# Performance work log

Measured on AMD Instinct MI355X. Metric: run time of the kernel, lower is better.

The kernel has to match this reference:

```python
import jax, jax.numpy as jnp
import numpy as np

B_, L, DM = 4, 1024, 1024
DI, DS, DR, DC = 1024, 16, 64, 4
NH = 4
DK = DM // NH


def setup_inputs() -> dict:
    key = jax.random.key(0)
    ks = jax.random.split(key, 16)
    def w(i, shape, scale=0.02):
        return jax.random.normal(ks[i], shape, dtype=jnp.float32) * scale
    inp = {
        "x": jax.random.normal(ks[0], (B_, L, DM), dtype=jnp.float32),
        "xx": jax.random.normal(ks[1], (B_, L, DI), dtype=jnp.float32),
        "in_proj_w": w(2, (DI, DM)),
        "conv_w": w(3, (DI, 1, DC)),            # depthwise conv, groups=DI
        "conv_b": jnp.zeros((DI,), jnp.float32),
        "x_proj_w": w(4, (DR + 2 * DS, DI)),
        "dt_proj_w": w(5, (DI, DR)),
        "dt_proj_b": jnp.zeros((DI,), jnp.float32),
        "A_log": jnp.log(jnp.tile(jnp.arange(1, DS + 1, dtype=jnp.float32)[None, :], (DI, 1))),
        "D": jnp.ones((DI,), jnp.float32),
        "wq": w(6, (DM, DM)), "bq": jnp.zeros((DM,), jnp.float32),
        "wk": w(7, (DM, DM)), "bk": jnp.zeros((DM,), jnp.float32),
        "wv": w(8, (DM, DM)), "bv": jnp.zeros((DM,), jnp.float32),
        "wo": w(9, (DM, DM)), "bo": jnp.zeros((DM,), jnp.float32),
    }
    return inp


def _stim_forward(x, xx, in_proj_w, conv_w, conv_b, x_proj_w, dt_proj_w, dt_proj_b,
                  A_log, D, wq, bq, wk, bk, wv, bv, wo, bo):
    b, l, _ = xx.shape
    # query branch: in_proj (Linear, no bias)
    q = x @ in_proj_w.T                                    # (b, l, DI)
    # kv branch: causal depthwise conv1d (padding d_conv-1, truncated to l)
    xc = jnp.transpose(xx, (0, 2, 1))                      # (b, DI, l)
    xc = jax.lax.conv_general_dilated(
        xc, conv_w, window_strides=(1,), padding=[(DC - 1, 0)],
        dimension_numbers=("NCH", "OIH", "NCH"), feature_group_count=DI)
    xc = xc + conv_b[None, :, None]
    u = jax.nn.silu(jnp.transpose(xc, (0, 2, 1)))          # (b, l, DI)
    # SSM parameter projections
    A = -jnp.exp(A_log)                                    # (DI, DS)
    x_dbl = u @ x_proj_w.T                                 # (b, l, DR+2*DS)
    delta, Bm, Cm = jnp.split(x_dbl, [DR, DR + DS], axis=-1)
    delta = jax.nn.softplus(delta @ dt_proj_w.T + dt_proj_b)  # (b, l, DI)
    deltaA = jnp.exp(jnp.einsum("bld,dn->bldn", delta, A))    # (b, l, DI, DS)
    deltaBu = jnp.einsum("bld,bln,bld->bldn", delta, Bm, u)   # (b, l, DI, DS)
    # selective scan over time
    def step(h, inp):
        dA_t, dBu_t, C_t = inp
        h = dA_t * h + dBu_t                               # (b, DI, DS)
        y_t = jnp.einsum("bdn,bn->bd", h, C_t)             # (b, DI)
        return h, y_t
    h0 = jnp.zeros((b, DI, DS), dtype=u.dtype)
    _, ys = jax.lax.scan(step, h0, (jnp.moveaxis(deltaA, 1, 0),
                                    jnp.moveaxis(deltaBu, 1, 0),
                                    jnp.moveaxis(Cm, 1, 0)))
    y = jnp.moveaxis(ys, 0, 1) + u * D                     # (b, l, DI)
    # cross attention: query = q, key/value = y
    Q = (q @ wq.T + bq).reshape(b, l, NH, DK).transpose(0, 2, 1, 3)
    K = (y @ wk.T + bk).reshape(b, l, NH, DK).transpose(0, 2, 1, 3)
    V = (y @ wv.T + bv).reshape(b, l, NH, DK).transpose(0, 2, 1, 3)
    scale = 1.0 / np.sqrt(DK).astype(np.float32)
    scores = jnp.einsum("bhqd,bhkd->bhqk", Q, K) * scale
    attn = jax.nn.softmax(scores, axis=-1)
    out = jnp.einsum("bhqk,bhkd->bhqd", attn, V)
    out = out.transpose(0, 2, 1, 3).reshape(b, l, DM)
    return out @ wo.T + bo


def reference(x, xx, in_proj_w, conv_w, conv_b, x_proj_w, dt_proj_w, dt_proj_b,
              A_log, D, wq, bq, wk, bk, wv, bv, wo, bo):
    return _stim_forward(x, xx, in_proj_w, conv_w, conv_b, x_proj_w, dt_proj_w,
                         dt_proj_b, A_log, D, wq, bq, wk, bk, wv, bv, wo, bo)
```

## Files before the change

kernel.cpp:

```cpp
#include <hip/hip_runtime.h>
#include <math.h>

#define B_  4
#define L_  1024
#define DM  1024
#define DI  1024
#define DS  16
#define DR  64
#define DCV 4
#define NH  4
#define DK  256

#define NCH 32
#define CHL (L_ / NCH)

typedef __attribute__((ext_vector_type(8))) short short8;
typedef __attribute__((ext_vector_type(4))) float floatx4;

static __device__ __forceinline__ unsigned short f2bf(float f) {
    unsigned int u = __float_as_uint(f);
    u += 0x7fffu + ((u >> 16) & 1u);
    return (unsigned short)(u >> 16);
}
static __device__ __forceinline__ float bf2f(unsigned short s) {
    return __uint_as_float(((unsigned int)s) << 16);
}

struct PrepArgs {
    const float* xx; const float* cw; const float* cb;
    float* u; unsigned short* ub;
    const float* xs; unsigned short* xd;
    const float* s[7]; unsigned short* d[7];
    int n[7];
    int ns[7];
};

__global__ __launch_bounds__(256) void prep(PrepArgs pa)
{
    int bid = blockIdx.x, tid = threadIdx.x;
    if (bid < 16384) {
        int idx = bid * 256 + tid;
        int d = idx & (DI - 1);
        int l = (idx >> 10) & (L_ - 1);
        int b = idx >> 20;
        const float* xb = pa.xx + (size_t)b * L_ * DI + d;
        float z = pa.cb[d];
#pragma unroll
        for (int j = 0; j < DCV; j++) {
            int t = l - (DCV - 1) + j;
            if (t >= 0) z += xb[(size_t)t * DI] * pa.cw[d * DCV + j];
        }
        float v = z / (1.0f + __expf(-z));
        pa.u[idx] = v;
        pa.ub[idx] = f2bf(v);
        return;
    }
    bid -= 16384;
    if (bid < 4096) {
        int i = (bid * 256 + tid) * 4;
        float4 v = *(const float4*)(pa.xs + i);
        ushort4 o;
        o.x = f2bf(v.x); o.y = f2bf(v.y); o.z = f2bf(v.z); o.w = f2bf(v.w);
        *(ushort4*)(pa.xd + i) = o;
        return;
    }
    bid -= 4096;
#pragma unroll
    for (int r = 0; r < 7; r++) {
        int nb = pa.n[r] >> 10;
        if (bid < nb) {
            int i = (bid * 256 + tid) * 4;
            int ns = pa.ns[r];
            const float* s = pa.s[r];
            ushort4 o;
            if (i + 4 <= ns) {
                float4 v = *(const float4*)(s + i);
                o.x = f2bf(v.x); o.y = f2bf(v.y); o.z = f2bf(v.z); o.w = f2bf(v.w);
            } else {
                float v[4];
#pragma unroll
                for (int j = 0; j < 4; j++) v[j] = (i + j < ns) ? s[i + j] : 0.f;
                o.x = f2bf(v[0]); o.y = f2bf(v[1]); o.z = f2bf(v[2]); o.w = f2bf(v[3]);
            }
            *(ushort4*)(pa.d[r] + i) = o;
            return;
        }
        bid -= nb;
    }
}

struct GDesc {
    const unsigned short* A;
    const unsigned short* W;
    const float* bias;
    float* Cf;
    unsigned short* Cb;
    int K, lda, ldw, ldc, ldc2;
    int mode;
    float scale;
    int gx, gy;
};
struct GArgs { GDesc g[3]; };

__global__ __launch_bounds__(256) void gemm_multi(GArgs ga)
{
    GDesc g = ga.g[blockIdx.z];
    if ((int)blockIdx.x >= g.gx || (int)blockIdx.y >= g.gy) return;

    __shared__ __align__(16) unsigned short Asm[128 * 32];
    __shared__ __align__(16) unsigned short Bsm[128 * 32];

    int tid = threadIdx.x;
    int wid = tid >> 6;
    int lane = tid & 63;
    int wm = wid & 1, wn = wid >> 1;
    int lr = lane & 15, quad = lane >> 4;

    const unsigned short* Ab = g.A + (size_t)blockIdx.y * 128 * g.lda;
    const unsigned short* Wb = g.W + (size_t)blockIdx.x * 128 * g.ldw;

    int srow = tid >> 2;
    int scol = (tid & 3) * 8;
    const unsigned short* Ap = Ab + (size_t)srow * g.lda + scol;
    const unsigned short* Wp = Wb + (size_t)srow * g.ldw + scol;

    unsigned short* lA0 = &Asm[(wid * 16) * 32];
    unsigned short* lA1 = &Asm[(64 + wid * 16) * 32];
    unsigned short* lB0 = &Bsm[(wid * 16) * 32];
    unsigned short* lB1 = &Bsm[(64 + wid * 16) * 32];

    floatx4 acc[4][4];
#pragma unroll
    for (int i = 0; i < 4; i++)
#pragma unroll
        for (int j = 0; j < 4; j++) acc[i][j] = (floatx4){0.f, 0.f, 0.f, 0.f};

#define GLL(gp, lp) __builtin_amdgcn_global_load_lds( \
        (const __attribute__((address_space(1))) void*)(gp), \
        (__attribute__((address_space(3))) void*)(lp), 16, 0, 0)

    for (int k0 = 0; k0 < g.K; k0 += 32) {
        GLL(Ap, lA0);
        GLL(Ap + (size_t)64 * g.lda, lA1);
        GLL(Wp, lB0);
        GLL(Wp + (size_t)64 * g.ldw, lB1);
        Ap += 32; Wp += 32;
        __syncthreads();

        short8 af[4], bf[4];
#pragma unroll
        for (int mt = 0; mt < 4; mt++)
            af[mt] = *(const short8*)&Asm[(wm * 64 + mt * 16 + lr) * 32 + quad * 8];
#pragma unroll
        for (int nt = 0; nt < 4; nt++)
            bf[nt] = *(const short8*)&Bsm[(wn * 64 + nt * 16 + lr) * 32 + quad * 8];
#pragma unroll
        for (int mt = 0; mt < 4; mt++)
#pragma unroll
            for (int nt = 0; nt < 4; nt++)
                acc[mt][nt] = __builtin_amdgcn_mfma_f32_16x16x32_bf16(
                    af[mt], bf[nt], acc[mt][nt], 0, 0, 0);
        __syncthreads();
    }
#undef GLL

    int bm = blockIdx.y * 128, bn = blockIdx.x * 128;
    int m = g.mode & 3;
#pragma unroll
    for (int mt = 0; mt < 4; mt++) {
#pragma unroll
        for (int nt = 0; nt < 4; nt++) {
            int row0 = bm + wm * 64 + mt * 16 + quad * 4;
            int col = bn + wn * 64 + nt * 16 + lr;
            float bv = g.bias ? g.bias[col] : 0.f;
#pragma unroll
            for (int i = 0; i < 4; i++) {
                float v = acc[mt][nt][i] * g.scale + bv;
                if (g.mode & 4) v = (v > 15.f) ? v : log1pf(__expf(v));
                if (m == 0) {
                    g.Cf[(size_t)(row0 + i) * g.ldc + col] = v;
                } else if (m == 1) {
                    g.Cb[(size_t)(row0 + i) * g.ldc + col] = f2bf(v);
                } else {
                    g.Cf[(size_t)(row0 + i) * g.ldc + col] = v;
                    g.Cb[(size_t)(row0 + i) * g.ldc2 + col] = f2bf(v);
                }
            }
        }
    }
}

__global__ __launch_bounds__(256) void gemm_batched(
    const unsigned short* __restrict__ A, const unsigned short* __restrict__ W,
    unsigned short* __restrict__ C,
    int K, int lda, int ldw, int ldc,
    long long sA1, long long sA2, long long sW1, long long sW2,
    long long sC1, long long sC2, float scale)
{
    __shared__ __align__(16) unsigned short Asm[128 * 32];
    __shared__ __align__(16) unsigned short Bsm[128 * 32];

    int z = blockIdx.z;
    long long bq = z >> 2, hq = z & 3;
    int tid = threadIdx.x;
    int wid = tid >> 6;
    int lane = tid & 63;
    int wm = wid & 1, wn = wid >> 1;
    int lr = lane & 15, quad = lane >> 4;

    const unsigned short* Ab = A + bq * sA1 + hq * sA2 + (size_t)blockIdx.y * 128 * lda;
    const unsigned short* Wb = W + bq * sW1 + hq * sW2 + (size_t)blockIdx.x * 128 * ldw;

    int srow = tid >> 2;
    int scol = (tid & 3) * 8;
    const unsigned short* Ap = Ab + (size_t)srow * lda + scol;
    const unsigned short* Wp = Wb + (size_t)srow * ldw + scol;

    unsigned short* lA0 = &Asm[(wid * 16) * 32];
    unsigned short* lA1 = &Asm[(64 + wid * 16) * 32];
    unsigned short* lB0 = &Bsm[(wid * 16) * 32];
    unsigned short* lB1 = &Bsm[(64 + wid * 16) * 32];

    floatx4 acc[4][4];
#pragma unroll
    for (int i = 0; i < 4; i++)
#pragma unroll
        for (int j = 0; j < 4; j++) acc[i][j] = (floatx4){0.f, 0.f, 0.f, 0.f};

#define GLL(gp, lp) __builtin_amdgcn_global_load_lds( \
        (const __attribute__((address_space(1))) void*)(gp), \
        (__attribute__((address_space(3))) void*)(lp), 16, 0, 0)

    for (int k0 = 0; k0 < K; k0 += 32) {
        GLL(Ap, lA0);
        GLL(Ap + (size_t)64 * lda, lA1);
        GLL(Wp, lB0);
        GLL(Wp + (size_t)64 * ldw, lB1);
        Ap += 32; Wp += 32;
        __syncthreads();

        short8 af[4], bf[4];
#pragma unroll
        for (int mt = 0; mt < 4; mt++)
            af[mt] = *(const short8*)&Asm[(wm * 64 + mt * 16 + lr) * 32 + quad * 8];
#pragma unroll
        for (int nt = 0; nt < 4; nt++)
            bf[nt] = *(const short8*)&Bsm[(wn * 64 + nt * 16 + lr) * 32 + quad * 8];
#pragma unroll
        for (int mt = 0; mt < 4; mt++)
#pragma unroll
            for (int nt = 0; nt < 4; nt++)
                acc[mt][nt] = __builtin_amdgcn_mfma_f32_16x16x32_bf16(
                    af[mt], bf[nt], acc[mt][nt], 0, 0, 0);
        __syncthreads();
    }
#undef GLL

    long long coff = bq * sC1 + hq * sC2;
    int bm = blockIdx.y * 128, bn = blockIdx.x * 128;
    unsigned short* Cb = C + coff;

#pragma unroll
    for (int mt = 0; mt < 4; mt++) {
#pragma unroll
        for (int nt = 0; nt < 4; nt++) {
            int row0 = bm + wm * 64 + mt * 16 + quad * 4;
            int col = bn + wn * 64 + nt * 16 + lr;
#pragma unroll
            for (int i = 0; i < 4; i++)
                Cb[(size_t)(row0 + i) * ldc + col] = f2bf(acc[mt][nt][i] * scale);
        }
    }
}

__global__ __launch_bounds__(256) void scan_a(
    const float* __restrict__ delta, const float* __restrict__ u,
    const float* __restrict__ xdbl, const float* __restrict__ A_log,
    float* __restrict__ Hc, float* __restrict__ sumdv)
{
    int gid = blockIdx.x * 256 + threadIdx.x;
    int c = gid >> 12;
    int bd = gid & 4095;
    int b = bd >> 10, d = bd & 1023;

    float a[16];
#pragma unroll
    for (int j = 0; j < 4; j++) {
        float4 al = *(const float4*)(A_log + d * 16 + j * 4);
        a[j * 4 + 0] = -__expf(al.x); a[j * 4 + 1] = -__expf(al.y);
        a[j * 4 + 2] = -__expf(al.z); a[j * 4 + 3] = -__expf(al.w);
    }
    float h[16];
#pragma unroll
    for (int n = 0; n < 16; n++) h[n] = 0.f;
    float sd = 0.f;

    int t0 = c * CHL;
    const float* dp = delta + ((size_t)(b * L_) + t0) * DI + d;
    const float* up = u + ((size_t)(b * L_) + t0) * DI + d;
    const float* xp = xdbl + ((size_t)(b * L_) + t0) * 128;

#pragma unroll 4
    for (int t = 0; t < CHL; t++) {
        float dv = dp[t * DI];
        float uv = up[t * DI];
        float duv = dv * uv;
        sd += dv;
        float Bv[16];
#pragma unroll
        for (int j = 0; j < 4; j++) {
            float4 bq = *(const float4*)(xp + t * 128 + 64 + j * 4);
            Bv[j * 4 + 0] = bq.x; Bv[j * 4 + 1] = bq.y;
            Bv[j * 4 + 2] = bq.z; Bv[j * 4 + 3] = bq.w;
        }
#pragma unroll
        for (int n = 0; n < 16; n++)
            h[n] = __expf(dv * a[n]) * h[n] + duv * Bv[n];
    }

    float* hp = Hc + ((size_t)c * 4096 + bd) * 16;
#pragma unroll
    for (int j = 0; j < 4; j++)
        *(float4*)(hp + j * 4) = make_float4(h[j * 4], h[j * 4 + 1], h[j * 4 + 2], h[j * 4 + 3]);
    sumdv[c * 4096 + bd] = sd;
}

__global__ __launch_bounds__(256) void scan_b(
    float* __restrict__ Hc, const float* __restrict__ sumdv,
    const float* __restrict__ A_log)
{
    int bd = blockIdx.x * 256 + threadIdx.x;
    int d = bd & 1023;

    float a[16];
#pragma unroll
    for (int j = 0; j < 4; j++) {
        float4 al = *(const float4*)(A_log + d * 16 + j * 4);
        a[j * 4 + 0] = -__expf(al.x); a[j * 4 + 1] = -__expf(al.y);
        a[j * 4 + 2] = -__expf(al.z); a[j * 4 + 3] = -__expf(al.w);
    }
    float H[16];
#pragma unroll
    for (int n = 0; n < 16; n++) H[n] = 0.f;

    for (int c = 0; c < NCH; c++) {
        float* hp = Hc + ((size_t)c * 4096 + bd) * 16;
        float sdv = sumdv[c * 4096 + bd];
        float hc[16];
#pragma unroll
        for (int j = 0; j < 4; j++) {
            float4 q = *(const float4*)(hp + j * 4);
            hc[j * 4 + 0] = q.x; hc[j * 4 + 1] = q.y; hc[j * 4 + 2] = q.z; hc[j * 4 + 3] = q.w;
        }
#pragma unroll
        for (int j = 0; j < 4; j++)
            *(float4*)(hp + j * 4) = make_float4(H[j * 4], H[j * 4 + 1], H[j * 4 + 2], H[j * 4 + 3]);
#pragma unroll
        for (int n = 0; n < 16; n++)
            H[n] = __expf(a[n] * sdv) * H[n] + hc[n];
    }
}

__global__ __launch_bounds__(256) void scan_c(
    const float* __restrict__ delta, const float* __restrict__ u,
    const float* __restrict__ xdbl, const float* __restrict__ A_log,
    const float* __restrict__ Dv, const float* __restrict__ Hstart,
    unsigned short* __restrict__ y)
{
    int gid = blockIdx.x * 256 + threadIdx.x;
    int c = gid >> 12;
    int bd = gid & 4095;
    int b = bd >> 10, d = bd & 1023;

    float a[16];
#pragma unroll
    for (int j = 0; j < 4; j++) {
        float4 al = *(const float4*)(A_log + d * 16 + j * 4);
        a[j * 4 + 0] = -__expf(al.x); a[j * 4 + 1] = -__expf(al.y);
        a[j * 4 + 2] = -__expf(al.z); a[j * 4 + 3] = -__expf(al.w);
    }
    float h[16];
    const float* hp = Hstart + ((size_t)c * 4096 + bd) * 16;
#pragma unroll
    for (int j = 0; j < 4; j++) {
        float4 q = *(const float4*)(hp + j * 4);
        h[j * 4 + 0] = q.x; h[j * 4 + 1] = q.y; h[j * 4 + 2] = q.z; h[j * 4 + 3] = q.w;
    }
    float Dd = Dv[d];

    int t0 = c * CHL;
    const float* dp = delta + ((size_t)(b * L_) + t0) * DI + d;
    const float* up = u + ((size_t)(b * L_) + t0) * DI + d;
    const float* xp = xdbl + ((size_t)(b * L_) + t0) * 128;
    unsigned short* yp = y + ((size_t)(b * L_) + t0) * DI + d;

#pragma unroll 4
    for (int t = 0; t < CHL; t++) {
        float dv = dp[t * DI];
        float uv = up[t * DI];
        float duv = dv * uv;
        float Bv[16], Cv[16];
#pragma unroll
        for (int j = 0; j < 4; j++) {
            float4 bq = *(const float4*)(xp + t * 128 + 64 + j * 4);
            Bv[j * 4 + 0] = bq.x; Bv[j * 4 + 1] = bq.y;
            Bv[j * 4 + 2] = bq.z; Bv[j * 4 + 3] = bq.w;
            float4 cq = *(const float4*)(xp + t * 128 + 80 + j * 4);
            Cv[j * 4 + 0] = cq.x; Cv[j * 4 + 1] = cq.y;
            Cv[j * 4 + 2] = cq.z; Cv[j * 4 + 3] = cq.w;
        }
        float ys = 0.f;
#pragma unroll
        for (int n = 0; n < 16; n++) {
            h[n] = __expf(dv * a[n]) * h[n] + duv * Bv[n];
            ys += h[n] * Cv[n];
        }
        yp[t * DI] = f2bf(ys + uv * Dd);
    }
}

__global__ __launch_bounds__(256) void softmax_rows(unsigned short* __restrict__ S)
{
    int row = blockIdx.x * 4 + (threadIdx.x >> 6);
    int lane = threadIdx.x & 63;
    unsigned short* p = S + (size_t)row * 1024;

    float v[16];
#pragma unroll
    for (int ch = 0; ch < 4; ch++) {
        ushort4 u4 = *(const ushort4*)(p + ch * 256 + lane * 4);
        v[ch * 4 + 0] = bf2f(u4.x); v[ch * 4 + 1] = bf2f(u4.y);
        v[ch * 4 + 2] = bf2f(u4.z); v[ch * 4 + 3] = bf2f(u4.w);
    }
    float m = -1e30f;
#pragma unroll
    for (int i = 0; i < 16; i++) m = fmaxf(m, v[i]);
#pragma unroll
    for (int off = 32; off >= 1; off >>= 1) m = fmaxf(m, __shfl_xor(m, off));
    float s = 0.f;
#pragma unroll
    for (int i = 0; i < 16; i++) { v[i] = __expf(v[i] - m); s += v[i]; }
#pragma unroll
    for (int off = 32; off >= 1; off >>= 1) s += __shfl_xor(s, off);
    float inv = 1.0f / s;
#pragma unroll
    for (int ch = 0; ch < 4; ch++) {
        ushort4 o;
        o.x = f2bf(v[ch * 4 + 0] * inv); o.y = f2bf(v[ch * 4 + 1] * inv);
        o.z = f2bf(v[ch * 4 + 2] * inv); o.w = f2bf(v[ch * 4 + 3] * inv);
        *(ushort4*)(p + ch * 256 + lane * 4) = o;
    }
}

__global__ __launch_bounds__(256) void transpose_v(
    const unsigned short* __restrict__ V, unsigned short* __restrict__ VT)
{
    __shared__ unsigned short tl[32][36];
    int bh = blockIdx.z;
    int b = bh >> 2, h = bh & 3;
    int l0 = blockIdx.x * 32, d0 = blockIdx.y * 32;
    int tid = threadIdx.x;
    int r = tid >> 3, c4 = (tid & 7) * 4;

    const unsigned short* src = V + ((size_t)(b * L_ + l0 + r)) * 1024 + h * DK + d0 + c4;
    ushort4 v = *(const ushort4*)src;
    tl[r][c4 + 0] = v.x; tl[r][c4 + 1] = v.y; tl[r][c4 + 2] = v.z; tl[r][c4 + 3] = v.w;
    __syncthreads();

    unsigned short* dst = VT + ((size_t)bh * DK + d0 + r) * L_ + l0 + c4;
    ushort4 o;
    o.x = tl[c4 + 0][r]; o.y = tl[c4 + 1][r]; o.z = tl[c4 + 2][r]; o.w = tl[c4 + 3][r];
    *(ushort4*)dst = o;
}

extern "C" void kernel_launch(void* const* d_in, const int* in_sizes, int n_in,
                              void* d_out, int out_size, void* d_ws, size_t ws_size,
                              hipStream_t stream)
{
    const float* x         = (const float*)d_in[0];
    const float* xx        = (const float*)d_in[1];
    const float* in_proj_w = (const float*)d_in[2];
    const float* conv_w    = (const float*)d_in[3];
    const float* conv_b    = (const float*)d_in[4];
    const float* x_proj_w  = (const float*)d_in[5];
    const float* dt_proj_w = (const float*)d_in[6];
    const float* dt_proj_b = (const float*)d_in[7];
    const float* A_log     = (const float*)d_in[8];
    const float* Dvec      = (const float*)d_in[9];
    const float* wq        = (const float*)d_in[10];
    const float* bq        = (const float*)d_in[11];
    const float* wk        = (const float*)d_in[12];
    const float* bk        = (const float*)d_in[13];
    const float* wv        = (const float*)d_in[14];
    const float* bv        = (const float*)d_in[15];
    const float* wo        = (const float*)d_in[16];
    const float* bo        = (const float*)d_in[17];
    float* out = (float*)d_out;

    char* w = (char*)d_ws;
    const size_t MB = 1024 * 1024, KB = 1024;
    float*          u_f    = (float*)(w + 0);
    float*          delta  = (float*)(w + 16 * MB);
    unsigned short* Sbuf   = (unsigned short*)(w + 0);
    unsigned short* x_bf   = (unsigned short*)(w + 32 * MB);
    unsigned short* Q_bf   = x_bf;
    unsigned short* q_bf   = (unsigned short*)(w + 40 * MB);
    unsigned short* VT     = q_bf;
    unsigned short* y_bf   = (unsigned short*)(w + 48 * MB);
    unsigned short* AO     = y_bf;
    unsigned short* K_bf   = (unsigned short*)(w + 56 * MB);
    unsigned short* V_bf   = (unsigned short*)(w + 64 * MB);
    unsigned short* u_bf   = (unsigned short*)(w + 72 * MB);
    float*          Hc     = (float*)(w + 72 * MB);
    float*          xdbl   = (float*)(w + 80 * MB);
    unsigned short* xdblb  = (unsigned short*)(w + 82 * MB);
    unsigned short* w_in   = (unsigned short*)(w + 83 * MB);
    unsigned short* w_q    = (unsigned short*)(w + 85 * MB);
    unsigned short* w_k    = (unsigned short*)(w + 87 * MB);
    unsigned short* w_v    = (unsigned short*)(w + 89 * MB);
    unsigned short* w_o    = (unsigned short*)(w + 91 * MB);
    unsigned short* w_xp   = (unsigned short*)(w + 93 * MB);
    unsigned short* w_dt   = (unsigned short*)(w + 93 * MB + 256 * KB);
    float*          sumdv  = (float*)(w + 93 * MB + 384 * KB);

    dim3 blk(256);
    const long long LL = L_;

    PrepArgs pa;
    pa.xx = xx; pa.cw = conv_w; pa.cb = conv_b; pa.u = u_f; pa.ub = u_bf;
    pa.xs = x; pa.xd = x_bf;
    pa.s[0] = in_proj_w; pa.d[0] = w_in; pa.n[0] = 1048576; pa.ns[0] = 1048576;
    pa.s[1] = wq;        pa.d[1] = w_q;  pa.n[1] = 1048576; pa.ns[1] = 1048576;
    pa.s[2] = wk;        pa.d[2] = w_k;  pa.n[2] = 1048576; pa.ns[2] = 1048576;
    pa.s[3] = wv;        pa.d[3] = w_v;  pa.n[3] = 1048576; pa.ns[3] = 1048576;
    pa.s[4] = wo;        pa.d[4] = w_o;  pa.n[4] = 1048576; pa.ns[4] = 1048576;
    pa.s[5] = x_proj_w;  pa.d[5] = w_xp; pa.n[5] = 131072;  pa.ns[5] = 98304;
    pa.s[6] = dt_proj_w; pa.d[6] = w_dt; pa.n[6] = 65536;   pa.ns[6] = 65536;
    prep<<<dim3(25792), blk, 0, stream>>>(pa);

    {
        GArgs ga = {};
        ga.g[0] = (GDesc){x_bf, w_in, nullptr, nullptr, q_bf,
                          1024, 1024, 1024, 1024, 0, 1, 1.0f, 8, 32};
        ga.g[1] = (GDesc){u_bf, w_xp, nullptr, xdbl, xdblb,
                          1024, 1024, 1024, 128, 128, 2, 1.0f, 1, 32};
        gemm_multi<<<dim3(8, 32, 2), blk, 0, stream>>>(ga);
    }
    {
        GArgs ga = {};
        ga.g[0] = (GDesc){xdblb, w_dt, dt_proj_b, delta, nullptr,
                          64, 128, 64, 1024, 0, 0 | 4, 1.0f, 8, 32};
        gemm_multi<<<dim3(8, 32, 1), blk, 0, stream>>>(ga);
    }
    scan_a<<<dim3(512), blk, 0, stream>>>(delta, u_f, xdbl, A_log, Hc, sumdv);
    scan_b<<<dim3(16), blk, 0, stream>>>(Hc, sumdv, A_log);
    scan_c<<<dim3(512), blk, 0, stream>>>(delta, u_f, xdbl, A_log, Dvec, Hc, y_bf);

    {
        GArgs ga = {};
        ga.g[0] = (GDesc){q_bf, w_q, bq, nullptr, Q_bf, 1024, 1024, 1024, 1024, 0, 1, 1.0f, 8, 32};
        ga.g[1] = (GDesc){y_bf, w_k, bk, nullptr, K_bf, 1024, 1024, 1024, 1024, 0, 1, 1.0f, 8, 32};
        ga.g[2] = (GDesc){y_bf, w_v, bv, nullptr, V_bf, 1024, 1024, 1024, 1024, 0, 1, 1.0f, 8, 32};
        gemm_multi<<<dim3(8, 32, 3), blk, 0, stream>>>(ga);
    }
    gemm_batched<<<dim3(8, 8, 16), blk, 0, stream>>>(Q_bf, K_bf, Sbuf,
        DK, 1024, 1024, 1024,
        LL * 1024, 256, LL * 1024, 256,
        4 * LL * 1024, LL * 1024, 0.0625f);
    softmax_rows<<<dim3(4096), blk, 0, stream>>>(Sbuf);
    transpose_v<<<dim3(32, 8, 16), blk, 0, stream>>>(V_bf, VT);
    gemm_batched<<<dim3(2, 8, 16), blk, 0, stream>>>(Sbuf, VT, AO,
        1024, 1024, 1024, 1024,
        4 * LL * 1024, LL * 1024,
        4 * (long long)DK * 1024, (long long)DK * 1024,
        LL * 1024, 256, 1.0f);
    {
        GArgs ga = {};
        ga.g[0] = (GDesc){AO, w_o, bo, out, nullptr, 1024, 1024, 1024, 1024, 0, 0, 1.0f, 8, 32};
        gemm_multi<<<dim3(8, 32, 1), blk, 0, stream>>>(ga);
    }
}
```

Baseline: 438.5 us.

## Fold in_proj into wq, use bf16 scan inputs, fuse softmax with V transpose

Precomputes the combined weight wq·in_proj (transposing in_proj in prep) so Q is computed directly from x, removing the separate 4096x1024x1024 in_proj GEMM and leaving only a small 1024^3 weight-product GEMM. Scan kernels now read u and B/C as bf16 instead of fp32 copies, which removes the fp32 u and xdbl writes and halves scan read traffic. Softmax and the V transpose are merged into one launch. Folding the weights and reading bf16 scan inputs change rounding and could shift accuracy.

```diff
diff --git a/kernel.cpp b/kernel.cpp
--- a/kernel.cpp
+++ b/kernel.cpp
@@ -28,15 +28,17 @@
 
 struct PrepArgs {
     const float* xx; const float* cw; const float* cb;
-    float* u; unsigned short* ub;
+    unsigned short* ub;
     const float* xs; unsigned short* xd;
-    const float* s[7]; unsigned short* d[7];
-    int n[7];
-    int ns[7];
+    const float* ipw; unsigned short* ipt;
+    const float* s[6]; unsigned short* d[6];
+    int n[6];
+    int ns[6];
 };
 
 __global__ __launch_bounds__(256) void prep(PrepArgs pa)
 {
+    __shared__ float tl[32][33];
     int bid = blockIdx.x, tid = threadIdx.x;
     if (bid < 16384) {
         int idx = bid * 256 + tid;
@@ -51,7 +53,6 @@
             if (t >= 0) z += xb[(size_t)t * DI] * pa.cw[d * DCV + j];
         }
         float v = z / (1.0f + __expf(-z));
-        pa.u[idx] = v;
         pa.ub[idx] = f2bf(v);
         return;
     }
@@ -65,8 +66,25 @@
         return;
     }
     bid -= 4096;
-#pragma unroll
-    for (int r = 0; r < 7; r++) {
+    if (bid < 1024) {
+        int ti = bid >> 5, tj = bid & 31;
+        int i0 = ti * 32, j0 = tj * 32;
+        int r = tid >> 3, c4 = (tid & 7) * 4;
+        const float* src = pa.ipw + (size_t)(i0 + r) * 1024 + j0 + c4;
+        float4 v = *(const float4*)src;
+        tl[r][c4 + 0] = v.x; tl[r][c4 + 1] = v.y;
+        tl[r][c4 + 2] = v.z; tl[r][c4 + 3] = v.w;
+        __syncthreads();
+        unsigned short* dst = pa.ipt + (size_t)(j0 + r) * 1024 + i0 + c4;
+        ushort4 o;
+        o.x = f2bf(tl[c4 + 0][r]); o.y = f2bf(tl[c4 + 1][r]);
+        o.z = f2bf(tl[c4 + 2][r]); o.w = f2bf(tl[c4 + 3][r]);
+        *(ushort4*)dst = o;
+        return;
+    }
+    bid -= 1024;
+#pragma unroll
+    for (int r = 0; r < 6; r++) {
         int nb = pa.n[r] >> 10;
         if (bid < nb) {
             int i = (bid * 256 + tid) * 4;
@@ -177,14 +195,8 @@
             for (int i = 0; i < 4; i++) {
                 float v = acc[mt][nt][i] * g.scale + bv;
                 if (g.mode & 4) v = (v > 15.f) ? v : log1pf(__expf(v));
-                if (m == 0) {
-                    g.Cf[(size_t)(row0 + i) * g.ldc + col] = v;
-                } else if (m == 1) {
-                    g.Cb[(size_t)(row0 + i) * g.ldc + col] = f2bf(v);
-                } else {
-                    g.Cf[(size_t)(row0 + i) * g.ldc + col] = v;
-                    g.Cb[(size_t)(row0 + i) * g.ldc2 + col] = f2bf(v);
-                }
+                if (m == 0) g.Cf[(size_t)(row0 + i) * g.ldc + col] = v;
+                else        g.Cb[(size_t)(row0 + i) * g.ldc + col] = f2bf(v);
             }
         }
     }
@@ -274,8 +286,8 @@
 }
 
 __global__ __launch_bounds__(256) void scan_a(
-    const float* __restrict__ delta, const float* __restrict__ u,
-    const float* __restrict__ xdbl, const float* __restrict__ A_log,
+    const float* __restrict__ delta, const unsigned short* __restrict__ u,
+    const unsigned short* __restrict__ xdbl, const float* __restrict__ A_log,
     float* __restrict__ Hc, float* __restrict__ sumdv)
 {
     int gid = blockIdx.x * 256 + threadIdx.x;
@@ -297,21 +309,22 @@
 
     int t0 = c * CHL;
     const float* dp = delta + ((size_t)(b * L_) + t0) * DI + d;
-    const float* up = u + ((size_t)(b * L_) + t0) * DI + d;
-    const float* xp = xdbl + ((size_t)(b * L_) + t0) * 128;
+    const unsigned short* up = u + ((size_t)(b * L_) + t0) * DI + d;
+    const unsigned short* xp = xdbl + ((size_t)(b * L_) + t0) * 128;
 
 #pragma unroll 4
     for (int t = 0; t < CHL; t++) {
         float dv = dp[t * DI];
-        float uv = up[t * DI];
+        float uv = bf2f(up[t * DI]);
         float duv = dv * uv;
         sd += dv;
+        short8 b0 = *(const short8*)(xp + t * 128 + 64);
+        short8 b1 = *(const short8*)(xp + t * 128 + 72);
         float Bv[16];
 #pragma unroll
-        for (int j = 0; j < 4; j++) {
-            float4 bq = *(const float4*)(xp + t * 128 + 64 + j * 4);
-            Bv[j * 4 + 0] = bq.x; Bv[j * 4 + 1] = bq.y;
-            Bv[j * 4 + 2] = bq.z; Bv[j * 4 + 3] = bq.w;
+        for (int j = 0; j < 8; j++) {
+            Bv[j] = bf2f((unsigned short)b0[j]);
+            Bv[8 + j] = bf2f((unsigned short)b1[j]);
         }
 #pragma unroll
         for (int n = 0; n < 16; n++)
@@ -362,8 +375,8 @@
 }
 
 __global__ __launch_bounds__(256) void scan_c(
-    const float* __restrict__ delta, const float* __restrict__ u,
-    const float* __restrict__ xdbl, const float* __restrict__ A_log,
+    const float* __restrict__ delta, const unsigned short* __restrict__ u,
+    const unsigned short* __restrict__ xdbl, const float* __restrict__ A_log,
     const float* __restrict__ Dv, const float* __restrict__ Hstart,
     unsigned short* __restrict__ y)
 {
@@ -390,24 +403,26 @@
 
     int t0 = c * CHL;
     const float* dp = delta + ((size_t)(b * L_) + t0) * DI + d;
-    const float* up = u + ((size_t)(b * L_) + t0) * DI + d;
-    const float* xp = xdbl + ((size_t)(b * L_) + t0) * 128;
+    const unsigned short* up = u + ((size_t)(b * L_) + t0) * DI + d;
+    const unsigned short* xp = xdbl + ((size_t)(b * L_) + t0) * 128;
     unsigned short* yp = y + ((size_t)(b * L_) + t0) * DI + d;
 
 #pragma unroll 4
     for (int t = 0; t < CHL; t++) {
         float dv = dp[t * DI];
-        float uv = up[t * DI];
+        float uv = bf2f(up[t * DI]);
         float duv = dv * uv;
+        short8 b0 = *(const short8*)(xp + t * 128 + 64);
+        short8 b1 = *(const short8*)(xp + t * 128 + 72);
+        short8 c0 = *(const short8*)(xp + t * 128 + 80);
+        short8 c1 = *(const short8*)(xp + t * 128 + 88);
         float Bv[16], Cv[16];
 #pragma unroll
-        for (int j = 0; j < 4; j++) {
-            float4 bq = *(const float4*)(xp + t * 128 + 64 + j * 4);
-            Bv[j * 4 + 0] = bq.x; Bv[j * 4 + 1] = bq.y;
-            Bv[j * 4 + 2] = bq.z; Bv[j * 4 + 3] = bq.w;
-            float4 cq = *(const float4*)(xp + t * 128 + 80 + j * 4);
-            Cv[j * 4 + 0] = cq.x; Cv[j * 4 + 1] = cq.y;
-            Cv[j * 4 + 2] = cq.z; Cv[j * 4 + 3] = cq.w;
+        for (int j = 0; j < 8; j++) {
+            Bv[j] = bf2f((unsigned short)b0[j]);
+            Bv[8 + j] = bf2f((unsigned short)b1[j]);
+            Cv[j] = bf2f((unsigned short)c0[j]);
+            Cv[8 + j] = bf2f((unsigned short)c1[j]);
         }
         float ys = 0.f;
 #pragma unroll
@@ -419,47 +434,47 @@
     }
 }
 
-__global__ __launch_bounds__(256) void softmax_rows(unsigned short* __restrict__ S)
-{
-    int row = blockIdx.x * 4 + (threadIdx.x >> 6);
-    int lane = threadIdx.x & 63;
-    unsigned short* p = S + (size_t)row * 1024;
-
-    float v[16];
-#pragma unroll
-    for (int ch = 0; ch < 4; ch++) {
-        ushort4 u4 = *(const ushort4*)(p + ch * 256 + lane * 4);
-        v[ch * 4 + 0] = bf2f(u4.x); v[ch * 4 + 1] = bf2f(u4.y);
-        v[ch * 4 + 2] = bf2f(u4.z); v[ch * 4 + 3] = bf2f(u4.w);
-    }
-    float m = -1e30f;
-#pragma unroll
-    for (int i = 0; i < 16; i++) m = fmaxf(m, v[i]);
-#pragma unroll
-    for (int off = 32; off >= 1; off >>= 1) m = fmaxf(m, __shfl_xor(m, off));
-    float s = 0.f;
-#pragma unroll
-    for (int i = 0; i < 16; i++) { v[i] = __expf(v[i] - m); s += v[i]; }
-#pragma unroll
-    for (int off = 32; off >= 1; off >>= 1) s += __shfl_xor(s, off);
-    float inv = 1.0f / s;
-#pragma unroll
-    for (int ch = 0; ch < 4; ch++) {
-        ushort4 o;
-        o.x = f2bf(v[ch * 4 + 0] * inv); o.y = f2bf(v[ch * 4 + 1] * inv);
-        o.z = f2bf(v[ch * 4 + 2] * inv); o.w = f2bf(v[ch * 4 + 3] * inv);
-        *(ushort4*)(p + ch * 256 + lane * 4) = o;
-    }
-}
-
-__global__ __launch_bounds__(256) void transpose_v(
-    const unsigned short* __restrict__ V, unsigned short* __restrict__ VT)
+__global__ __launch_bounds__(256) void post_s(
+    unsigned short* __restrict__ S, const unsigned short* __restrict__ V,
+    unsigned short* __restrict__ VT)
 {
     __shared__ unsigned short tl[32][36];
-    int bh = blockIdx.z;
+    int bid = blockIdx.x, tid = threadIdx.x;
+    if (bid < 4096) {
+        int row = bid * 4 + (tid >> 6);
+        int lane = tid & 63;
+        unsigned short* p = S + (size_t)row * 1024;
+        float v[16];
+#pragma unroll
+        for (int ch = 0; ch < 4; ch++) {
+            ushort4 u4 = *(const ushort4*)(p + ch * 256 + lane * 4);
+            v[ch * 4 + 0] = bf2f(u4.x); v[ch * 4 + 1] = bf2f(u4.y);
+            v[ch * 4 + 2] = bf2f(u4.z); v[ch * 4 + 3] = bf2f(u4.w);
+        }
+        float m = -1e30f;
+#pragma unroll
+        for (int i = 0; i < 16; i++) m = fmaxf(m, v[i]);
+#pragma unroll
+        for (int off = 32; off >= 1; off >>= 1) m = fmaxf(m, __shfl_xor(m, off));
+        float s = 0.f;
+#pragma unroll
+        for (int i = 0; i < 16; i++) { v[i] = __expf(v[i] - m); s += v[i]; }
+#pragma unroll
+        for (int off = 32; off >= 1; off >>= 1) s += __shfl_xor(s, off);
+        float inv = 1.0f / s;
+#pragma unroll
+        for (int ch = 0; ch < 4; ch++) {
+            ushort4 o;
+            o.x = f2bf(v[ch * 4 + 0] * inv); o.y = f2bf(v[ch * 4 + 1] * inv);
+            o.z = f2bf(v[ch * 4 + 2] * inv); o.w = f2bf(v[ch * 4 + 3] * inv);
+            *(ushort4*)(p + ch * 256 + lane * 4) = o;
+        }
+        return;
+    }
+    bid -= 4096;
+    int lx = bid & 31, dy = (bid >> 5) & 7, bh = bid >> 8;
     int b = bh >> 2, h = bh & 3;
-    int l0 = blockIdx.x * 32, d0 = blockIdx.y * 32;
-    int tid = threadIdx.x;
+    int l0 = lx * 32, d0 = dy * 32;
     int r = tid >> 3, c4 = (tid & 7) * 4;
 
     const unsigned short* src = V + ((size_t)(b * L_ + l0 + r)) * 1024 + h * DK + d0 + c4;
@@ -499,22 +514,20 @@
 
     char* w = (char*)d_ws;
     const size_t MB = 1024 * 1024, KB = 1024;
-    float*          u_f    = (float*)(w + 0);
+    float*          Hc     = (float*)(w + 0);
     float*          delta  = (float*)(w + 16 * MB);
     unsigned short* Sbuf   = (unsigned short*)(w + 0);
     unsigned short* x_bf   = (unsigned short*)(w + 32 * MB);
-    unsigned short* Q_bf   = x_bf;
-    unsigned short* q_bf   = (unsigned short*)(w + 40 * MB);
-    unsigned short* VT     = q_bf;
+    unsigned short* Q_bf   = (unsigned short*)(w + 40 * MB);
     unsigned short* y_bf   = (unsigned short*)(w + 48 * MB);
     unsigned short* AO     = y_bf;
     unsigned short* K_bf   = (unsigned short*)(w + 56 * MB);
     unsigned short* V_bf   = (unsigned short*)(w + 64 * MB);
     unsigned short* u_bf   = (unsigned short*)(w + 72 * MB);
-    float*          Hc     = (float*)(w + 72 * MB);
-    float*          xdbl   = (float*)(w + 80 * MB);
+    unsigned short* VT     = u_bf;
+    unsigned short* w_qc   = (unsigned short*)(w + 80 * MB);
     unsigned short* xdblb  = (unsigned short*)(w + 82 * MB);
-    unsigned short* w_in   = (unsigned short*)(w + 83 * MB);
+    unsigned short* w_inT  = (unsigned short*)(w + 83 * MB);
     unsigned short* w_q    = (unsigned short*)(w + 85 * MB);
     unsigned short* w_k    = (unsigned short*)(w + 87 * MB);
     unsigned short* w_v    = (unsigned short*)(w + 89 * MB);
@@ -527,23 +540,23 @@
     const long long LL = L_;
 
     PrepArgs pa;
-    pa.xx = xx; pa.cw = conv_w; pa.cb = conv_b; pa.u = u_f; pa.ub = u_bf;
+    pa.xx = xx; pa.cw = conv_w; pa.cb = conv_b; pa.ub = u_bf;
     pa.xs = x; pa.xd = x_bf;
-    pa.s[0] = in_proj_w; pa.d[0] = w_in; pa.n[0] = 1048576; pa.ns[0] = 1048576;
-    pa.s[1] = wq;        pa.d[1] = w_q;  pa.n[1] = 1048576; pa.ns[1] = 1048576;
-    pa.s[2] = wk;        pa.d[2] = w_k;  pa.n[2] = 1048576; pa.ns[2] = 1048576;
-    pa.s[3] = wv;        pa.d[3] = w_v;  pa.n[3] = 1048576; pa.ns[3] = 1048576;
-    pa.s[4] = wo;        pa.d[4] = w_o;  pa.n[4] = 1048576; pa.ns[4] = 1048576;
-    pa.s[5] = x_proj_w;  pa.d[5] = w_xp; pa.n[5] = 131072;  pa.ns[5] = 98304;
-    pa.s[6] = dt_proj_w; pa.d[6] = w_dt; pa.n[6] = 65536;   pa.ns[6] = 65536;
+    pa.ipw = in_proj_w; pa.ipt = w_inT;
+    pa.s[0] = wq;        pa.d[0] = w_q;  pa.n[0] = 1048576; pa.ns[0] = 1048576;
+    pa.s[1] = wk;        pa.d[1] = w_k;  pa.n[1] = 1048576; pa.ns[1] = 1048576;
+    pa.s[2] = wv;        pa.d[2] = w_v;  pa.n[2] = 1048576; pa.ns[2] = 1048576;
+    pa.s[3] = wo;        pa.d[3] = w_o;  pa.n[3] = 1048576; pa.ns[3] = 1048576;
+    pa.s[4] = x_proj_w;  pa.d[4] = w_xp; pa.n[4] = 131072;  pa.ns[4] = 98304;
+    pa.s[5] = dt_proj_w; pa.d[5] = w_dt; pa.n[5] = 65536;   pa.ns[5] = 65536;
     prep<<<dim3(25792), blk, 0, stream>>>(pa);
 
     {
         GArgs ga = {};
-        ga.g[0] = (GDesc){x_bf, w_in, nullptr, nullptr, q_bf,
-                          1024, 1024, 1024, 1024, 0, 1, 1.0f, 8, 32};
-        ga.g[1] = (GDesc){u_bf, w_xp, nullptr, xdbl, xdblb,
-                          1024, 1024, 1024, 128, 128, 2, 1.0f, 1, 32};
+        ga.g[0] = (GDesc){u_bf, w_xp, nullptr, nullptr, xdblb,
+                          1024, 1024, 1024, 128, 0, 1, 1.0f, 1, 32};
+        ga.g[1] = (GDesc){w_q, w_inT, nullptr, nullptr, w_qc,
+                          1024, 1024, 1024, 1024, 0, 1, 1.0f, 8, 8};
         gemm_multi<<<dim3(8, 32, 2), blk, 0, stream>>>(ga);
     }
     {
@@ -552,13 +565,13 @@
                           64, 128, 64, 1024, 0, 0 | 4, 1.0f, 8, 32};
         gemm_multi<<<dim3(8, 32, 1), blk, 0, stream>>>(ga);
     }
-    scan_a<<<dim3(512), blk, 0, stream>>>(delta, u_f, xdbl, A_log, Hc, sumdv);
+    scan_a<<<dim3(512), blk, 0, stream>>>(delta, u_bf, xdblb, A_log, Hc, sumdv);
     scan_b<<<dim3(16), blk, 0, stream>>>(Hc, sumdv, A_log);
-    scan_c<<<dim3(512), blk, 0, stream>>>(delta, u_f, xdbl, A_log, Dvec, Hc, y_bf);
+    scan_c<<<dim3(512), blk, 0, stream>>>(delta, u_bf, xdblb, A_log, Dvec, Hc, y_bf);
 
     {
         GArgs ga = {};
-        ga.g[0] = (GDesc){q_bf, w_q, bq, nullptr, Q_bf, 1024, 1024, 1024, 1024, 0, 1, 1.0f, 8, 32};
+        ga.g[0] = (GDesc){x_bf, w_qc, bq, nullptr, Q_bf, 1024, 1024, 1024, 1024, 0, 1, 1.0f, 8, 32};
         ga.g[1] = (GDesc){y_bf, w_k, bk, nullptr, K_bf, 1024, 1024, 1024, 1024, 0, 1, 1.0f, 8, 32};
         ga.g[2] = (GDesc){y_bf, w_v, bv, nullptr, V_bf, 1024, 1024, 1024, 1024, 0, 1, 1.0f, 8, 32};
         gemm_multi<<<dim3(8, 32, 3), blk, 0, stream>>>(ga);
@@ -567,8 +580,7 @@
         DK, 1024, 1024, 1024,
         LL * 1024, 256, LL * 1024, 256,
         4 * LL * 1024, LL * 1024, 0.0625f);
-    softmax_rows<<<dim3(4096), blk, 0, stream>>>(Sbuf);
-    transpose_v<<<dim3(32, 8, 16), blk, 0, stream>>>(V_bf, VT);
+    post_s<<<dim3(8192), blk, 0, stream>>>(Sbuf, V_bf, VT);
     gemm_batched<<<dim3(2, 8, 16), blk, 0, stream>>>(Sbuf, VT, AO,
         1024, 1024, 1024, 1024,
         4 * LL * 1024, LL * 1024,
```

Measured after the change: 487.7 us. 11.2% more time.
